# Kernel tuning notes

Measured on AMD Instinct MI355X. Metric: run time of the kernel, lower is better.

The kernel has to match this reference:

```python
import jax, jax.numpy as jnp
import numpy as np

N = 50000   # nodes
E = 800000  # edges
H = 128     # hidden_dim
R = 20      # num_rbf
LN_EPS = 1e-5


def setup_inputs() -> dict:
    key = jax.random.key(0)
    ks = jax.random.split(key, 16)
    rn = lambda k, shape, scale=1.0: (jax.random.normal(k, shape, dtype=jnp.float32) * scale)
    s = rn(ks[0], (N, H))
    v = rn(ks[1], (N, 3, H))
    edge_index = jax.random.randint(ks[2], (2, E), 0, N, dtype=jnp.int32)
    edge_rbf = jax.random.uniform(ks[3], (E, R), dtype=jnp.float32)
    ev = rn(ks[4], (E, 3))
    edge_vec_unit = ev / jnp.linalg.norm(ev, axis=-1, keepdims=True)
    # message_net: Linear(H+R -> H), SiLU, Linear(H -> 3H)
    mW1 = rn(ks[5], (H + R, H), (H + R) ** -0.5)
    mb1 = jnp.zeros((H,), jnp.float32)
    mW2 = rn(ks[6], (H, 3 * H), H ** -0.5)
    mb2 = jnp.zeros((3 * H,), jnp.float32)
    # update_net: Linear(2H -> H), SiLU, Linear(H -> 2H)
    uW1 = rn(ks[7], (2 * H, H), (2 * H) ** -0.5)
    ub1 = jnp.zeros((H,), jnp.float32)
    uW2 = rn(ks[8], (H, 2 * H), H ** -0.5)
    ub2 = jnp.zeros((2 * H,), jnp.float32)
    ln_g = jnp.ones((H,), jnp.float32)
    ln_b = jnp.zeros((H,), jnp.float32)
    return {"s": s, "v": v, "edge_rbf": edge_rbf, "edge_vec_unit": edge_vec_unit,
            "mW1": mW1, "mb1": mb1, "mW2": mW2, "mb2": mb2,
            "uW1": uW1, "ub1": ub1, "uW2": uW2, "ub2": ub2,
            "ln_g": ln_g, "ln_b": ln_b, "edge_index": edge_index}


def reference(s, v, edge_rbf, edge_vec_unit, mW1, mb1, mW2, mb2,
              uW1, ub1, uW2, ub2, ln_g, ln_b, edge_index):
    src, dst = edge_index[0], edge_index[1]
    n = s.shape[0]
    # message net on gathered scalar features + rbf: [E, H+R] -> [E, 3H]
    x = jnp.concatenate([s[src], edge_rbf], axis=-1)
    phi = jax.nn.silu(x @ mW1 + mb1) @ mW2 + mb2
    a_ss, a_sv, a_vv = jnp.split(phi, 3, axis=-1)  # each [E, H]
    # vector messages: [E, 3, H]
    msg_v = a_sv[:, None, :] * edge_vec_unit[:, :, None] + a_vv[:, None, :] * v[src]
    # scatter-add aggregation to destination nodes
    agg_s = jax.ops.segment_sum(a_ss, dst, num_segments=n)      # [N, H]
    agg_v = jax.ops.segment_sum(msg_v, dst, num_segments=n)     # [N, 3, H]
    v_new = v + agg_v
    v_norm = jnp.sqrt(jnp.sum(v_new * v_new, axis=1))           # [N, H]
    upd_in = jnp.concatenate([s + agg_s, v_norm], axis=-1)      # [N, 2H]
    update = jax.nn.silu(upd_in @ uW1 + ub1) @ uW2 + ub2        # [N, 2H]
    delta_s, gate_v = jnp.split(update, 2, axis=-1)
    # layer norm over last dim (biased variance, as torch LayerNorm)
    y = s + delta_s
    mu = jnp.mean(y, axis=-1, keepdims=True)
    var = jnp.mean((y - mu) ** 2, axis=-1, keepdims=True)
    s_out = (y - mu) * jax.lax.rsqrt(var + LN_EPS) * ln_g + ln_b
    v_out = gate_v[:, None, :] * v_new
    return s_out, v_out
```

## Files before the change

### kernel.cpp

```cpp
#include <hip/hip_runtime.h>
#include <hip/hip_bf16.h>
#include <math.h>


#define H 128
#define R 20
#define KX (H + R)
#define LN_EPS 1e-5f

#define BE 64
#define XS_STRIDE 149
#define H1_STRIDE 129

#define BN 64
#define US_STRIDE 257
#define H2_STRIDE 129

__device__ __forceinline__ float silu_f(float x) {
    return x / (1.0f + __expf(-x));
}

__global__ __launch_bounds__(256)
void zero_f4_kernel(float4* __restrict__ p, long n4)
{
    const long stride = (long)gridDim.x * blockDim.x;
    for (long i = (long)blockIdx.x * blockDim.x + threadIdx.x; i < n4; i += stride)
        p[i] = make_float4(0.f, 0.f, 0.f, 0.f);
}

__global__ __launch_bounds__(256)
void zero_i_kernel(int* __restrict__ p, int n)
{
    const int stride = gridDim.x * blockDim.x;
    for (int i = blockIdx.x * blockDim.x + threadIdx.x; i < n; i += stride)
        p[i] = 0;
}

__global__ __launch_bounds__(256)
void hist_kernel(const int* __restrict__ eidx, int E, int* __restrict__ cnt)
{
    const int stride = gridDim.x * blockDim.x;
    for (int i = blockIdx.x * blockDim.x + threadIdx.x; i < E; i += stride)
        atomicAdd(&cnt[eidx[E + i]], 1);
}

__global__ __launch_bounds__(1024, 1)
void scan_kernel(const int* __restrict__ cnt, int N, int* __restrict__ fill)
{
    __shared__ int lds[1024];
    __shared__ int base_s;
    const int tid = threadIdx.x;
    if (tid == 0) base_s = 0;
    __syncthreads();
    const int nchunk = (N + 1023) >> 10;
    for (int c = 0; c < nchunk; ++c) {
        const int i   = (c << 10) + tid;
        const int val = (i < N) ? cnt[i] : 0;
        lds[tid] = val;
        __syncthreads();
        for (int off = 1; off < 1024; off <<= 1) {
            int t = (tid >= off) ? lds[tid - off] : 0;
            __syncthreads();
            lds[tid] += t;
            __syncthreads();
        }
        const int incl = lds[tid];
        if (i < N) fill[i] = base_s + (incl - val);
        __syncthreads();
        if (tid == 1023) base_s += incl;
        __syncthreads();
    }
}

__global__ __launch_bounds__(256)
void scatter_kernel(const int* __restrict__ eidx, int E,
                    int* __restrict__ fill, int* __restrict__ sorted)
{
    const int stride = gridDim.x * blockDim.x;
    for (int i = blockIdx.x * blockDim.x + threadIdx.x; i < E; i += stride) {
        const int d    = eidx[E + i];
        const int slot = atomicAdd(&fill[d], 1);
        sorted[slot] = i;
    }
}

__global__ __launch_bounds__(256, 2)
void painn_edge_kernel(const float* __restrict__ s,
                       const float* __restrict__ v,
                       const float* __restrict__ rbf,
                       const float* __restrict__ evu,
                       const float* __restrict__ mW1,
                       const float* __restrict__ mb1,
                       const float* __restrict__ mW2,
                       const float* __restrict__ mb2,
                       const int*   __restrict__ eidx,
                       const int*   __restrict__ sorted,
                       int E,
                       float* __restrict__ agg_s,
                       float* __restrict__ agg_v)
{
    __shared__ float Xs[BE * XS_STRIDE];
    __shared__ float H1s[BE * H1_STRIDE];
    __shared__ float evus[BE][3];
    __shared__ int   eids[BE];
    __shared__ int   srcs[BE];
    __shared__ int   dsts[BE];

    const int t  = threadIdx.x;
    const int e0 = blockIdx.x * BE;

    if (t < BE) {
        const int e = sorted[e0 + t];
        eids[t] = e;
        srcs[t] = eidx[e];
        dsts[t] = eidx[E + e];
    }
    __syncthreads();

    if (t < BE * 3) {
        int r = t / 3, c = t - r * 3;
        evus[r][c] = evu[eids[r] * 3 + c];
    }

    #pragma unroll
    for (int it = 0; it < 8; ++it) {
        int idx = t + it * 256;
        int row = idx >> 5;
        int c4  = (idx & 31) << 2;
        const float4 val = *reinterpret_cast<const float4*>(s + srcs[row] * H + c4);
        float* p = &Xs[row * XS_STRIDE + c4];
        p[0] = val.x; p[1] = val.y; p[2] = val.z; p[3] = val.w;
    }
    #pragma unroll
    for (int it = 0; it < 5; ++it) {
        int idx = t + it * 256;
        int row = idx / R;
        int c   = idx - row * R;
        Xs[row * XS_STRIDE + H + c] = rbf[eids[row] * R + c];
    }
    __syncthreads();

    const int ty = t >> 4;
    const int tx = t & 15;
    const int jb = tx << 3;
    const int er = ty << 2;

    const int rcol = t & 127;
    const int rr0  = (t >> 7) * 32;

    {
        float acc[4][8];
        #pragma unroll
        for (int r2 = 0; r2 < 4; ++r2)
            #pragma unroll
            for (int j = 0; j < 8; ++j) acc[r2][j] = 0.f;

        const float* wp = mW1 + jb;
        for (int k = 0; k < KX; ++k) {
            const float4 w0 = *reinterpret_cast<const float4*>(wp);
            const float4 w1 = *reinterpret_cast<const float4*>(wp + 4);
            wp += H;
            float xk[4];
            #pragma unroll
            for (int r2 = 0; r2 < 4; ++r2) xk[r2] = Xs[(er + r2) * XS_STRIDE + k];
            #pragma unroll
            for (int r2 = 0; r2 < 4; ++r2) {
                acc[r2][0] += xk[r2] * w0.x;
                acc[r2][1] += xk[r2] * w0.y;
                acc[r2][2] += xk[r2] * w0.z;
                acc[r2][3] += xk[r2] * w0.w;
                acc[r2][4] += xk[r2] * w1.x;
                acc[r2][5] += xk[r2] * w1.y;
                acc[r2][6] += xk[r2] * w1.z;
                acc[r2][7] += xk[r2] * w1.w;
            }
        }
        const float4 b0 = *reinterpret_cast<const float4*>(mb1 + jb);
        const float4 b1 = *reinterpret_cast<const float4*>(mb1 + jb + 4);
        const float bias[8] = {b0.x, b0.y, b0.z, b0.w, b1.x, b1.y, b1.z, b1.w};
        #pragma unroll
        for (int r2 = 0; r2 < 4; ++r2) {
            #pragma unroll
            for (int j = 0; j < 8; ++j) {
                float a = acc[r2][j] + bias[j];
                H1s[(er + r2) * H1_STRIDE + jb + j] = silu_f(a);
            }
        }
    }
    __syncthreads();

    {
        float acc[4][8];
        #pragma unroll
        for (int r2 = 0; r2 < 4; ++r2)
            #pragma unroll
            for (int j = 0; j < 8; ++j) acc[r2][j] = 0.f;

        const float* wp = mW2 + jb;
        for (int k = 0; k < H; ++k) {
            const float4 w0 = *reinterpret_cast<const float4*>(wp);
            const float4 w1 = *reinterpret_cast<const float4*>(wp + 4);
            wp += 3 * H;
            float hk[4];
            #pragma unroll
            for (int r2 = 0; r2 < 4; ++r2) hk[r2] = H1s[(er + r2) * H1_STRIDE + k];
            #pragma unroll
            for (int r2 = 0; r2 < 4; ++r2) {
                acc[r2][0] += hk[r2] * w0.x;
                acc[r2][1] += hk[r2] * w0.y;
                acc[r2][2] += hk[r2] * w0.z;
                acc[r2][3] += hk[r2] * w0.w;
                acc[r2][4] += hk[r2] * w1.x;
                acc[r2][5] += hk[r2] * w1.y;
                acc[r2][6] += hk[r2] * w1.z;
                acc[r2][7] += hk[r2] * w1.w;
            }
        }
        const float4 b0 = *reinterpret_cast<const float4*>(mb2 + jb);
        const float4 b1 = *reinterpret_cast<const float4*>(mb2 + jb + 4);
        const float bias[8] = {b0.x, b0.y, b0.z, b0.w, b1.x, b1.y, b1.z, b1.w};
        #pragma unroll
        for (int r2 = 0; r2 < 4; ++r2)
            #pragma unroll
            for (int j = 0; j < 8; ++j)
                Xs[(er + r2) * XS_STRIDE + jb + j] = acc[r2][j] + bias[j];
        __syncthreads();

        float run = 0.f;
        int prev = dsts[rr0];
        for (int r = rr0; r < rr0 + 32; ++r) {
            const int d = dsts[r];
            if (d != prev) {
                unsafeAtomicAdd(&agg_s[prev * H + rcol], run);
                run = 0.f; prev = d;
            }
            run += Xs[r * XS_STRIDE + rcol];
        }
        unsafeAtomicAdd(&agg_s[prev * H + rcol], run);
    }
    __syncthreads();

    {
        float asv[4][8], avv[4][8];
        #pragma unroll
        for (int r2 = 0; r2 < 4; ++r2)
            #pragma unroll
            for (int j = 0; j < 8; ++j) { asv[r2][j] = 0.f; avv[r2][j] = 0.f; }

        const float* wp = mW2 + H + jb;
        for (int k = 0; k < H; ++k) {
            const float4 s0 = *reinterpret_cast<const float4*>(wp);
            const float4 s1 = *reinterpret_cast<const float4*>(wp + 4);
            const float4 v0 = *reinterpret_cast<const float4*>(wp + H);
            const float4 v1 = *reinterpret_cast<const float4*>(wp + H + 4);
            wp += 3 * H;
            float hk[4];
            #pragma unroll
            for (int r2 = 0; r2 < 4; ++r2) hk[r2] = H1s[(er + r2) * H1_STRIDE + k];
            #pragma unroll
            for (int r2 = 0; r2 < 4; ++r2) {
                asv[r2][0] += hk[r2] * s0.x;  avv[r2][0] += hk[r2] * v0.x;
                asv[r2][1] += hk[r2] * s0.y;  avv[r2][1] += hk[r2] * v0.y;
                asv[r2][2] += hk[r2] * s0.z;  avv[r2][2] += hk[r2] * v0.z;
                asv[r2][3] += hk[r2] * s0.w;  avv[r2][3] += hk[r2] * v0.w;
                asv[r2][4] += hk[r2] * s1.x;  avv[r2][4] += hk[r2] * v1.x;
                asv[r2][5] += hk[r2] * s1.y;  avv[r2][5] += hk[r2] * v1.y;
                asv[r2][6] += hk[r2] * s1.z;  avv[r2][6] += hk[r2] * v1.z;
                asv[r2][7] += hk[r2] * s1.w;  avv[r2][7] += hk[r2] * v1.w;
            }
        }
        const float4 bs0 = *reinterpret_cast<const float4*>(mb2 + H + jb);
        const float4 bs1 = *reinterpret_cast<const float4*>(mb2 + H + jb + 4);
        const float4 bv0 = *reinterpret_cast<const float4*>(mb2 + 2 * H + jb);
        const float4 bv1 = *reinterpret_cast<const float4*>(mb2 + 2 * H + jb + 4);
        float msv[4][8], mvv[4][8];
        #pragma unroll
        for (int r2 = 0; r2 < 4; ++r2) {
            msv[r2][0] = asv[r2][0] + bs0.x;  mvv[r2][0] = avv[r2][0] + bv0.x;
            msv[r2][1] = asv[r2][1] + bs0.y;  mvv[r2][1] = avv[r2][1] + bv0.y;
            msv[r2][2] = asv[r2][2] + bs0.z;  mvv[r2][2] = avv[r2][2] + bv0.z;
            msv[r2][3] = asv[r2][3] + bs0.w;  mvv[r2][3] = avv[r2][3] + bv0.w;
            msv[r2][4] = asv[r2][4] + bs1.x;  mvv[r2][4] = avv[r2][4] + bv1.x;
            msv[r2][5] = asv[r2][5] + bs1.y;  mvv[r2][5] = avv[r2][5] + bv1.y;
            msv[r2][6] = asv[r2][6] + bs1.z;  mvv[r2][6] = avv[r2][6] + bv1.z;
            msv[r2][7] = asv[r2][7] + bs1.w;  mvv[r2][7] = avv[r2][7] + bv1.w;
        }

        #pragma unroll
        for (int d = 0; d < 3; ++d) {
            #pragma unroll
            for (int r2 = 0; r2 < 4; ++r2) {
                const int e  = er + r2;
                const int sn = srcs[e];
                const float ed = evus[e][d];
                const float* vp = v + (sn * 3 + d) * H + jb;
                const float4 vv0 = *reinterpret_cast<const float4*>(vp);
                const float4 vv1 = *reinterpret_cast<const float4*>(vp + 4);
                float* rp = &Xs[e * XS_STRIDE + jb];
                rp[0] = msv[r2][0] * ed + mvv[r2][0] * vv0.x;
                rp[1] = msv[r2][1] * ed + mvv[r2][1] * vv0.y;
                rp[2] = msv[r2][2] * ed + mvv[r2][2] * vv0.z;
                rp[3] = msv[r2][3] * ed + mvv[r2][3] * vv0.w;
                rp[4] = msv[r2][4] * ed + mvv[r2][4] * vv1.x;
                rp[5] = msv[r2][5] * ed + mvv[r2][5] * vv1.y;
                rp[6] = msv[r2][6] * ed + mvv[r2][6] * vv1.z;
                rp[7] = msv[r2][7] * ed + mvv[r2][7] * vv1.w;
            }
            __syncthreads();

            float run = 0.f;
            int prev = dsts[rr0];
            for (int r = rr0; r < rr0 + 32; ++r) {
                const int dn = dsts[r];
                if (dn != prev) {
                    unsafeAtomicAdd(&agg_v[(prev * 3 + d) * H + rcol], run);
                    run = 0.f; prev = dn;
                }
                run += Xs[r * XS_STRIDE + rcol];
            }
            unsafeAtomicAdd(&agg_v[(prev * 3 + d) * H + rcol], run);
            __syncthreads();
        }
    }
}

__global__ __launch_bounds__(256, 1)
void painn_node_kernel(const float* __restrict__ s,
                       const float* __restrict__ v,
                       const float* __restrict__ uW1,
                       const float* __restrict__ ub1,
                       const float* __restrict__ uW2,
                       const float* __restrict__ ub2,
                       const float* __restrict__ ln_g,
                       const float* __restrict__ ln_b,
                       int N,
                       float* __restrict__ out_s,
                       float* __restrict__ out_v)
{
    __shared__ float Us[BN * US_STRIDE];
    __shared__ float H2s[BN * H2_STRIDE];

    const int t  = threadIdx.x;
    const int n0 = blockIdx.x * BN;
    const int m  = min(BN, N - n0);

    #pragma unroll
    for (int it = 0; it < 8; ++it) {
        int idx = t + it * 256;
        int row = idx >> 5;
        int c4  = (idx & 31) << 2;
        if (row < m) {
            const int nb = (n0 + row) * H + c4;
            const float4 sv = *reinterpret_cast<const float4*>(s + nb);
            const float4 av = *reinterpret_cast<const float4*>(out_s + nb);
            float* p = &Us[row * US_STRIDE + c4];
            p[0] = sv.x + av.x; p[1] = sv.y + av.y;
            p[2] = sv.z + av.z; p[3] = sv.w + av.w;

            float nx = 0.f, ny = 0.f, nz = 0.f, nw = 0.f;
            #pragma unroll
            for (int d = 0; d < 3; ++d) {
                const int vb = ((n0 + row) * 3 + d) * H + c4;
                const float4 vv = *reinterpret_cast<const float4*>(v + vb);
                const float4 avv = *reinterpret_cast<const float4*>(out_v + vb);
                const float a0 = vv.x + avv.x, a1 = vv.y + avv.y;
                const float a2 = vv.z + avv.z, a3 = vv.w + avv.w;
                nx += a0 * a0; ny += a1 * a1; nz += a2 * a2; nw += a3 * a3;
            }
            float* q = &Us[row * US_STRIDE + H + c4];
            q[0] = sqrtf(nx); q[1] = sqrtf(ny); q[2] = sqrtf(nz); q[3] = sqrtf(nw);
        }
    }
    __syncthreads();

    const int ty = t >> 4;
    const int tx = t & 15;
    const int jb = tx << 3;
    const int nr = ty << 2;

    {
        float acc[4][8];
        #pragma unroll
        for (int r2 = 0; r2 < 4; ++r2)
            #pragma unroll
            for (int j = 0; j < 8; ++j) acc[r2][j] = 0.f;

        const float* wp = uW1 + jb;
        for (int k = 0; k < 2 * H; ++k) {
            const float4 w0 = *reinterpret_cast<const float4*>(wp);
            const float4 w1 = *reinterpret_cast<const float4*>(wp + 4);
            wp += H;
            float uk[4];
            #pragma unroll
            for (int r2 = 0; r2 < 4; ++r2) uk[r2] = Us[(nr + r2) * US_STRIDE + k];
            #pragma unroll
            for (int r2 = 0; r2 < 4; ++r2) {
                acc[r2][0] += uk[r2] * w0.x;
                acc[r2][1] += uk[r2] * w0.y;
                acc[r2][2] += uk[r2] * w0.z;
                acc[r2][3] += uk[r2] * w0.w;
                acc[r2][4] += uk[r2] * w1.x;
                acc[r2][5] += uk[r2] * w1.y;
                acc[r2][6] += uk[r2] * w1.z;
                acc[r2][7] += uk[r2] * w1.w;
            }
        }
        const float4 b0 = *reinterpret_cast<const float4*>(ub1 + jb);
        const float4 b1 = *reinterpret_cast<const float4*>(ub1 + jb + 4);
        const float bias[8] = {b0.x, b0.y, b0.z, b0.w, b1.x, b1.y, b1.z, b1.w};
        #pragma unroll
        for (int r2 = 0; r2 < 4; ++r2)
            #pragma unroll
            for (int j = 0; j < 8; ++j)
                H2s[(nr + r2) * H2_STRIDE + jb + j] = silu_f(acc[r2][j] + bias[j]);
    }
    __syncthreads();

    float gate[4][8];
    {
        float ad[4][8], ag[4][8];
        #pragma unroll
        for (int r2 = 0; r2 < 4; ++r2)
            #pragma unroll
            for (int j = 0; j < 8; ++j) { ad[r2][j] = 0.f; ag[r2][j] = 0.f; }

        const float* wp = uW2 + jb;
        for (int k = 0; k < H; ++k) {
            const float4 d0 = *reinterpret_cast<const float4*>(wp);
            const float4 d1 = *reinterpret_cast<const float4*>(wp + 4);
            const float4 g0 = *reinterpret_cast<const float4*>(wp + H);
            const float4 g1 = *reinterpret_cast<const float4*>(wp + H + 4);
            wp += 2 * H;
            float hk[4];
            #pragma unroll
            for (int r2 = 0; r2 < 4; ++r2) hk[r2] = H2s[(nr + r2) * H2_STRIDE + k];
            #pragma unroll
            for (int r2 = 0; r2 < 4; ++r2) {
                ad[r2][0] += hk[r2] * d0.x;  ag[r2][0] += hk[r2] * g0.x;
                ad[r2][1] += hk[r2] * d0.y;  ag[r2][1] += hk[r2] * g0.y;
                ad[r2][2] += hk[r2] * d0.z;  ag[r2][2] += hk[r2] * g0.z;
                ad[r2][3] += hk[r2] * d0.w;  ag[r2][3] += hk[r2] * g0.w;
                ad[r2][4] += hk[r2] * d1.x;  ag[r2][4] += hk[r2] * g1.x;
                ad[r2][5] += hk[r2] * d1.y;  ag[r2][5] += hk[r2] * g1.y;
                ad[r2][6] += hk[r2] * d1.z;  ag[r2][6] += hk[r2] * g1.z;
                ad[r2][7] += hk[r2] * d1.w;  ag[r2][7] += hk[r2] * g1.w;
            }
        }
        const float4 bd0 = *reinterpret_cast<const float4*>(ub2 + jb);
        const float4 bd1 = *reinterpret_cast<const float4*>(ub2 + jb + 4);
        const float4 bg0 = *reinterpret_cast<const float4*>(ub2 + H + jb);
        const float4 bg1 = *reinterpret_cast<const float4*>(ub2 + H + jb + 4);
        const float bd[8] = {bd0.x, bd0.y, bd0.z, bd0.w, bd1.x, bd1.y, bd1.z, bd1.w};
        const float bg[8] = {bg0.x, bg0.y, bg0.z, bg0.w, bg1.x, bg1.y, bg1.z, bg1.w};

        #pragma unroll
        for (int r2 = 0; r2 < 4; ++r2) {
            #pragma unroll
            for (int j = 0; j < 8; ++j) gate[r2][j] = ag[r2][j] + bg[j];
            if (nr + r2 < m) {
                const int nb = (n0 + nr + r2) * H + jb;
                const float4 s0 = *reinterpret_cast<const float4*>(s + nb);
                const float4 s1 = *reinterpret_cast<const float4*>(s + nb + 4);
                const float sl[8] = {s0.x, s0.y, s0.z, s0.w, s1.x, s1.y, s1.z, s1.w};
                float* yp = &Us[(nr + r2) * US_STRIDE + jb];
                #pragma unroll
                for (int j = 0; j < 8; ++j) yp[j] = sl[j] + ad[r2][j] + bd[j];
            }
        }
    }
    __syncthreads();

    {
        const int row = t >> 2;
        const int q   = t & 3;
        if (row < m) {
            float sum = 0.f, ss = 0.f;
            #pragma unroll
            for (int i = 0; i < 32; ++i) {
                const float val = Us[row * US_STRIDE + q * 32 + i];
                sum += val; ss += val * val;
            }
            sum += __shfl_xor(sum, 1); ss += __shfl_xor(ss, 1);
            sum += __shfl_xor(sum, 2); ss += __shfl_xor(ss, 2);
            const float mu   = sum * (1.0f / H);
            const float var  = ss * (1.0f / H) - mu * mu;
            const float rstd = rsqrtf(fmaxf(var, 0.f) + LN_EPS);
            #pragma unroll
            for (int i4 = 0; i4 < 8; ++i4) {
                const int c = q * 32 + i4 * 4;
                const float4 g = *reinterpret_cast<const float4*>(ln_g + c);
                const float4 b = *reinterpret_cast<const float4*>(ln_b + c);
                const float* yp = &Us[row * US_STRIDE + c];
                float4 o;
                o.x = (yp[0] - mu) * rstd * g.x + b.x;
                o.y = (yp[1] - mu) * rstd * g.y + b.y;
                o.z = (yp[2] - mu) * rstd * g.z + b.z;
                o.w = (yp[3] - mu) * rstd * g.w + b.w;
                *reinterpret_cast<float4*>(out_s + (n0 + row) * H + c) = o;
            }
        }
    }

    #pragma unroll
    for (int r2 = 0; r2 < 4; ++r2) {
        if (nr + r2 < m) {
            const int nn = n0 + nr + r2;
            #pragma unroll
            for (int d = 0; d < 3; ++d) {
                const int vb = (nn * 3 + d) * H + jb;
                const float4 vv0 = *reinterpret_cast<const float4*>(v + vb);
                const float4 vv1 = *reinterpret_cast<const float4*>(v + vb + 4);
                const float4 av0 = *reinterpret_cast<const float4*>(out_v + vb);
                const float4 av1 = *reinterpret_cast<const float4*>(out_v + vb + 4);
                float4 o0, o1;
                o0.x = gate[r2][0] * (vv0.x + av0.x);
                o0.y = gate[r2][1] * (vv0.y + av0.y);
                o0.z = gate[r2][2] * (vv0.z + av0.z);
                o0.w = gate[r2][3] * (vv0.w + av0.w);
                o1.x = gate[r2][4] * (vv1.x + av1.x);
                o1.y = gate[r2][5] * (vv1.y + av1.y);
                o1.z = gate[r2][6] * (vv1.z + av1.z);
                o1.w = gate[r2][7] * (vv1.w + av1.w);
                *reinterpret_cast<float4*>(out_v + vb)     = o0;
                *reinterpret_cast<float4*>(out_v + vb + 4) = o1;
            }
        }
    }
}

extern "C" void kernel_launch(void* const* d_in, const int* in_sizes, int n_in,
                              void* d_out, int out_size, void* d_ws, size_t ws_size,
                              hipStream_t stream)
{
    const float* s    = (const float*)d_in[0];
    const float* v    = (const float*)d_in[1];
    const float* rbf  = (const float*)d_in[2];
    const float* evu  = (const float*)d_in[3];
    const float* mW1  = (const float*)d_in[4];
    const float* mb1  = (const float*)d_in[5];
    const float* mW2  = (const float*)d_in[6];
    const float* mb2  = (const float*)d_in[7];
    const float* uW1  = (const float*)d_in[8];
    const float* ub1  = (const float*)d_in[9];
    const float* uW2  = (const float*)d_in[10];
    const float* ub2  = (const float*)d_in[11];
    const float* ln_g = (const float*)d_in[12];
    const float* ln_b = (const float*)d_in[13];
    const int*   eidx = (const int*)d_in[14];

    const int N = in_sizes[0] / H;
    const int E = in_sizes[2] / R;

    float* agg_s = (float*)d_out;
    float* agg_v = (float*)d_out + (size_t)N * H;

    int* cnt    = (int*)d_ws;
    int* fill   = cnt + N;
    int* sorted = fill + N;

    const long n4 = (long)N * 4 * H / 4;
    zero_f4_kernel<<<dim3(2048), dim3(256), 0, stream>>>((float4*)d_out, n4);
    zero_i_kernel<<<dim3(64), dim3(256), 0, stream>>>(cnt, N);

    hist_kernel<<<dim3(2048), dim3(256), 0, stream>>>(eidx, E, cnt);
    scan_kernel<<<dim3(1), dim3(1024), 0, stream>>>(cnt, N, fill);
    scatter_kernel<<<dim3(2048), dim3(256), 0, stream>>>(eidx, E, fill, sorted);

    painn_edge_kernel<<<dim3(E / BE), dim3(256), 0, stream>>>(
        s, v, rbf, evu, mW1, mb1, mW2, mb2, eidx, sorted, E, agg_s, agg_v);

    painn_node_kernel<<<dim3((N + BN - 1) / BN), dim3(256), 0, stream>>>(
        s, v, uW1, ub1, uW2, ub2, ln_g, ln_b, N, agg_s, agg_v);
}
```

Measured before the change: 2.519 ms.

## Double edge-kernel threads, shrink per-thread tile, vectorize shared-memory accesses

The edge kernel now runs 512 threads per block instead of 256. Each thread computes 2 edge rows instead of 4, and the segmented-reduction slices shrink from 32 to 16 rows, which lowers register pressure and allows more resident waves. Shared-memory strides are padded to multiples of 4/8 so float4 loads and stores of X/H1 rows are aligned, and the k loops read 4 activations at a time. The risk is that weight loads from global/L2 are amortized over fewer rows, and padding to aligned strides may bring back bank conflicts.

```diff
diff --git a/kernel.cpp b/kernel.cpp
--- a/kernel.cpp
+++ b/kernel.cpp
@@ -9,8 +9,8 @@
 #define LN_EPS 1e-5f
 
 #define BE 64
-#define XS_STRIDE 149
-#define H1_STRIDE 129
+#define XS_STRIDE 152
+#define H1_STRIDE 136
 
 #define BN 64
 #define US_STRIDE 257
@@ -84,7 +84,7 @@
     }
 }
 
-__global__ __launch_bounds__(256, 2)
+__global__ __launch_bounds__(512, 4)
 void painn_edge_kernel(const float* __restrict__ s,
                        const float* __restrict__ v,
                        const float* __restrict__ rbf,
@@ -123,112 +123,120 @@
     }
 
     #pragma unroll
-    for (int it = 0; it < 8; ++it) {
-        int idx = t + it * 256;
+    for (int it = 0; it < 4; ++it) {
+        int idx = t + it * 512;
         int row = idx >> 5;
         int c4  = (idx & 31) << 2;
         const float4 val = *reinterpret_cast<const float4*>(s + srcs[row] * H + c4);
-        float* p = &Xs[row * XS_STRIDE + c4];
-        p[0] = val.x; p[1] = val.y; p[2] = val.z; p[3] = val.w;
+        *reinterpret_cast<float4*>(&Xs[row * XS_STRIDE + c4]) = val;
     }
     #pragma unroll
-    for (int it = 0; it < 5; ++it) {
-        int idx = t + it * 256;
-        int row = idx / R;
-        int c   = idx - row * R;
-        Xs[row * XS_STRIDE + H + c] = rbf[eids[row] * R + c];
-    }
-    __syncthreads();
-
-    const int ty = t >> 4;
-    const int tx = t & 15;
-    const int jb = tx << 3;
-    const int er = ty << 2;
+    for (int it = 0; it < 3; ++it) {
+        int idx = t + it * 512;
+        if (idx < BE * R) {
+            int row = idx / R;
+            int c   = idx - row * R;
+            Xs[row * XS_STRIDE + H + c] = rbf[eids[row] * R + c];
+        }
+    }
+    __syncthreads();
+
+    const int ty  = t >> 4;
+    const int tx  = t & 15;
+    const int jb  = tx << 3;
+    const int er0 = ty << 1;
+    const int er1 = er0 + 1;
 
     const int rcol = t & 127;
-    const int rr0  = (t >> 7) * 32;
+    const int rr0  = (t >> 7) << 4;
 
     {
-        float acc[4][8];
-        #pragma unroll
-        for (int r2 = 0; r2 < 4; ++r2)
-            #pragma unroll
-            for (int j = 0; j < 8; ++j) acc[r2][j] = 0.f;
+        float acc0[8], acc1[8];
+        #pragma unroll
+        for (int j = 0; j < 8; ++j) { acc0[j] = 0.f; acc1[j] = 0.f; }
 
         const float* wp = mW1 + jb;
-        for (int k = 0; k < KX; ++k) {
-            const float4 w0 = *reinterpret_cast<const float4*>(wp);
-            const float4 w1 = *reinterpret_cast<const float4*>(wp + 4);
-            wp += H;
-            float xk[4];
-            #pragma unroll
-            for (int r2 = 0; r2 < 4; ++r2) xk[r2] = Xs[(er + r2) * XS_STRIDE + k];
-            #pragma unroll
-            for (int r2 = 0; r2 < 4; ++r2) {
-                acc[r2][0] += xk[r2] * w0.x;
-                acc[r2][1] += xk[r2] * w0.y;
-                acc[r2][2] += xk[r2] * w0.z;
-                acc[r2][3] += xk[r2] * w0.w;
-                acc[r2][4] += xk[r2] * w1.x;
-                acc[r2][5] += xk[r2] * w1.y;
-                acc[r2][6] += xk[r2] * w1.z;
-                acc[r2][7] += xk[r2] * w1.w;
-            }
+        for (int k = 0; k < KX; k += 4) {
+            const float4 xa = *reinterpret_cast<const float4*>(&Xs[er0 * XS_STRIDE + k]);
+            const float4 xb = *reinterpret_cast<const float4*>(&Xs[er1 * XS_STRIDE + k]);
+            const float xav[4] = {xa.x, xa.y, xa.z, xa.w};
+            const float xbv[4] = {xb.x, xb.y, xb.z, xb.w};
+            #pragma unroll
+            for (int kk = 0; kk < 4; ++kk) {
+                const float4 w0 = *reinterpret_cast<const float4*>(wp + kk * H);
+                const float4 w1 = *reinterpret_cast<const float4*>(wp + kk * H + 4);
+                const float wj[8] = {w0.x, w0.y, w0.z, w0.w, w1.x, w1.y, w1.z, w1.w};
+                #pragma unroll
+                for (int j = 0; j < 8; ++j) {
+                    acc0[j] += xav[kk] * wj[j];
+                    acc1[j] += xbv[kk] * wj[j];
+                }
+            }
+            wp += 4 * H;
         }
         const float4 b0 = *reinterpret_cast<const float4*>(mb1 + jb);
         const float4 b1 = *reinterpret_cast<const float4*>(mb1 + jb + 4);
         const float bias[8] = {b0.x, b0.y, b0.z, b0.w, b1.x, b1.y, b1.z, b1.w};
-        #pragma unroll
-        for (int r2 = 0; r2 < 4; ++r2) {
-            #pragma unroll
-            for (int j = 0; j < 8; ++j) {
-                float a = acc[r2][j] + bias[j];
-                H1s[(er + r2) * H1_STRIDE + jb + j] = silu_f(a);
-            }
-        }
+        float4 o0, o1;
+        o0.x = silu_f(acc0[0] + bias[0]); o0.y = silu_f(acc0[1] + bias[1]);
+        o0.z = silu_f(acc0[2] + bias[2]); o0.w = silu_f(acc0[3] + bias[3]);
+        o1.x = silu_f(acc0[4] + bias[4]); o1.y = silu_f(acc0[5] + bias[5]);
+        o1.z = silu_f(acc0[6] + bias[6]); o1.w = silu_f(acc0[7] + bias[7]);
+        *reinterpret_cast<float4*>(&H1s[er0 * H1_STRIDE + jb])     = o0;
+        *reinterpret_cast<float4*>(&H1s[er0 * H1_STRIDE + jb + 4]) = o1;
+        o0.x = silu_f(acc1[0] + bias[0]); o0.y = silu_f(acc1[1] + bias[1]);
+        o0.z = silu_f(acc1[2] + bias[2]); o0.w = silu_f(acc1[3] + bias[3]);
+        o1.x = silu_f(acc1[4] + bias[4]); o1.y = silu_f(acc1[5] + bias[5]);
+        o1.z = silu_f(acc1[6] + bias[6]); o1.w = silu_f(acc1[7] + bias[7]);
+        *reinterpret_cast<float4*>(&H1s[er1 * H1_STRIDE + jb])     = o0;
+        *reinterpret_cast<float4*>(&H1s[er1 * H1_STRIDE + jb + 4]) = o1;
     }
     __syncthreads();
 
     {
-        float acc[4][8];
-        #pragma unroll
-        for (int r2 = 0; r2 < 4; ++r2)
-            #pragma unroll
-            for (int j = 0; j < 8; ++j) acc[r2][j] = 0.f;
+        float acc0[8], acc1[8];
+        #pragma unroll
+        for (int j = 0; j < 8; ++j) { acc0[j] = 0.f; acc1[j] = 0.f; }
 
         const float* wp = mW2 + jb;
-        for (int k = 0; k < H; ++k) {
-            const float4 w0 = *reinterpret_cast<const float4*>(wp);
-            const float4 w1 = *reinterpret_cast<const float4*>(wp + 4);
-            wp += 3 * H;
-            float hk[4];
-            #pragma unroll
-            for (int r2 = 0; r2 < 4; ++r2) hk[r2] = H1s[(er + r2) * H1_STRIDE + k];
-            #pragma unroll
-            for (int r2 = 0; r2 < 4; ++r2) {
-                acc[r2][0] += hk[r2] * w0.x;
-                acc[r2][1] += hk[r2] * w0.y;
-                acc[r2][2] += hk[r2] * w0.z;
-                acc[r2][3] += hk[r2] * w0.w;
-                acc[r2][4] += hk[r2] * w1.x;
-                acc[r2][5] += hk[r2] * w1.y;
-                acc[r2][6] += hk[r2] * w1.z;
-                acc[r2][7] += hk[r2] * w1.w;
-            }
+        for (int k = 0; k < H; k += 4) {
+            const float4 ha = *reinterpret_cast<const float4*>(&H1s[er0 * H1_STRIDE + k]);
+            const float4 hb = *reinterpret_cast<const float4*>(&H1s[er1 * H1_STRIDE + k]);
+            const float hav[4] = {ha.x, ha.y, ha.z, ha.w};
+            const float hbv[4] = {hb.x, hb.y, hb.z, hb.w};
+            #pragma unroll
+            for (int kk = 0; kk < 4; ++kk) {
+                const float4 w0 = *reinterpret_cast<const float4*>(wp + kk * 3 * H);
+                const float4 w1 = *reinterpret_cast<const float4*>(wp + kk * 3 * H + 4);
+                const float wj[8] = {w0.x, w0.y, w0.z, w0.w, w1.x, w1.y, w1.z, w1.w};
+                #pragma unroll
+                for (int j = 0; j < 8; ++j) {
+                    acc0[j] += hav[kk] * wj[j];
+                    acc1[j] += hbv[kk] * wj[j];
+                }
+            }
+            wp += 4 * 3 * H;
         }
         const float4 b0 = *reinterpret_cast<const float4*>(mb2 + jb);
         const float4 b1 = *reinterpret_cast<const float4*>(mb2 + jb + 4);
-        const float bias[8] = {b0.x, b0.y, b0.z, b0.w, b1.x, b1.y, b1.z, b1.w};
-        #pragma unroll
-        for (int r2 = 0; r2 < 4; ++r2)
-            #pragma unroll
-            for (int j = 0; j < 8; ++j)
-                Xs[(er + r2) * XS_STRIDE + jb + j] = acc[r2][j] + bias[j];
+        float4 o0, o1;
+        o0.x = acc0[0] + b0.x; o0.y = acc0[1] + b0.y;
+        o0.z = acc0[2] + b0.z; o0.w = acc0[3] + b0.w;
+        o1.x = acc0[4] + b1.x; o1.y = acc0[5] + b1.y;
+        o1.z = acc0[6] + b1.z; o1.w = acc0[7] + b1.w;
+        *reinterpret_cast<float4*>(&Xs[er0 * XS_STRIDE + jb])     = o0;
+        *reinterpret_cast<float4*>(&Xs[er0 * XS_STRIDE + jb + 4]) = o1;
+        o0.x = acc1[0] + b0.x; o0.y = acc1[1] + b0.y;
+        o0.z = acc1[2] + b0.z; o0.w = acc1[3] + b0.w;
+        o1.x = acc1[4] + b1.x; o1.y = acc1[5] + b1.y;
+        o1.z = acc1[6] + b1.z; o1.w = acc1[7] + b1.w;
+        *reinterpret_cast<float4*>(&Xs[er1 * XS_STRIDE + jb])     = o0;
+        *reinterpret_cast<float4*>(&Xs[er1 * XS_STRIDE + jb + 4]) = o1;
         __syncthreads();
 
         float run = 0.f;
         int prev = dsts[rr0];
-        for (int r = rr0; r < rr0 + 32; ++r) {
+        for (int r = rr0; r < rr0 + 16; ++r) {
             const int d = dsts[r];
             if (d != prev) {
                 unsafeAtomicAdd(&agg_s[prev * H + rcol], run);
@@ -241,84 +249,92 @@
     __syncthreads();
 
     {
-        float asv[4][8], avv[4][8];
-        #pragma unroll
-        for (int r2 = 0; r2 < 4; ++r2)
-            #pragma unroll
-            for (int j = 0; j < 8; ++j) { asv[r2][j] = 0.f; avv[r2][j] = 0.f; }
+        float asv0[8], asv1[8], avv0[8], avv1[8];
+        #pragma unroll
+        for (int j = 0; j < 8; ++j) {
+            asv0[j] = 0.f; asv1[j] = 0.f; avv0[j] = 0.f; avv1[j] = 0.f;
+        }
 
         const float* wp = mW2 + H + jb;
-        for (int k = 0; k < H; ++k) {
-            const float4 s0 = *reinterpret_cast<const float4*>(wp);
-            const float4 s1 = *reinterpret_cast<const float4*>(wp + 4);
-            const float4 v0 = *reinterpret_cast<const float4*>(wp + H);
-            const float4 v1 = *reinterpret_cast<const float4*>(wp + H + 4);
-            wp += 3 * H;
-            float hk[4];
-            #pragma unroll
-            for (int r2 = 0; r2 < 4; ++r2) hk[r2] = H1s[(er + r2) * H1_STRIDE + k];
-            #pragma unroll
-            for (int r2 = 0; r2 < 4; ++r2) {
-                asv[r2][0] += hk[r2] * s0.x;  avv[r2][0] += hk[r2] * v0.x;
-                asv[r2][1] += hk[r2] * s0.y;  avv[r2][1] += hk[r2] * v0.y;
-                asv[r2][2] += hk[r2] * s0.z;  avv[r2][2] += hk[r2] * v0.z;
-                asv[r2][3] += hk[r2] * s0.w;  avv[r2][3] += hk[r2] * v0.w;
-                asv[r2][4] += hk[r2] * s1.x;  avv[r2][4] += hk[r2] * v1.x;
-                asv[r2][5] += hk[r2] * s1.y;  avv[r2][5] += hk[r2] * v1.y;
-                asv[r2][6] += hk[r2] * s1.z;  avv[r2][6] += hk[r2] * v1.z;
-                asv[r2][7] += hk[r2] * s1.w;  avv[r2][7] += hk[r2] * v1.w;
-            }
+        for (int k = 0; k < H; k += 2) {
+            const float2 ha = *reinterpret_cast<const float2*>(&H1s[er0 * H1_STRIDE + k]);
+            const float2 hb = *reinterpret_cast<const float2*>(&H1s[er1 * H1_STRIDE + k]);
+            const float hav[2] = {ha.x, ha.y};
+            const float hbv[2] = {hb.x, hb.y};
+            #pragma unroll
+            for (int kk = 0; kk < 2; ++kk) {
+                const float4 s0 = *reinterpret_cast<const float4*>(wp + kk * 3 * H);
+                const float4 s1 = *reinterpret_cast<const float4*>(wp + kk * 3 * H + 4);
+                const float4 v0 = *reinterpret_cast<const float4*>(wp + kk * 3 * H + H);
+                const float4 v1 = *reinterpret_cast<const float4*>(wp + kk * 3 * H + H + 4);
+                const float ws[8] = {s0.x, s0.y, s0.z, s0.w, s1.x, s1.y, s1.z, s1.w};
+                const float wv[8] = {v0.x, v0.y, v0.z, v0.w, v1.x, v1.y, v1.z, v1.w};
+                #pragma unroll
+                for (int j = 0; j < 8; ++j) {
+                    asv0[j] += hav[kk] * ws[j];  avv0[j] += hav[kk] * wv[j];
+                    asv1[j] += hbv[kk] * ws[j];  avv1[j] += hbv[kk] * wv[j];
+                }
+            }
+            wp += 2 * 3 * H;
         }
         const float4 bs0 = *reinterpret_cast<const float4*>(mb2 + H + jb);
         const float4 bs1 = *reinterpret_cast<const float4*>(mb2 + H + jb + 4);
         const float4 bv0 = *reinterpret_cast<const float4*>(mb2 + 2 * H + jb);
         const float4 bv1 = *reinterpret_cast<const float4*>(mb2 + 2 * H + jb + 4);
-        float msv[4][8], mvv[4][8];
-        #pragma unroll
-        for (int r2 = 0; r2 < 4; ++r2) {
-            msv[r2][0] = asv[r2][0] + bs0.x;  mvv[r2][0] = avv[r2][0] + bv0.x;
-            msv[r2][1] = asv[r2][1] + bs0.y;  mvv[r2][1] = avv[r2][1] + bv0.y;
-            msv[r2][2] = asv[r2][2] + bs0.z;  mvv[r2][2] = avv[r2][2] + bv0.z;
-            msv[r2][3] = asv[r2][3] + bs0.w;  mvv[r2][3] = avv[r2][3] + bv0.w;
-            msv[r2][4] = asv[r2][4] + bs1.x;  mvv[r2][4] = avv[r2][4] + bv1.x;
-            msv[r2][5] = asv[r2][5] + bs1.y;  mvv[r2][5] = avv[r2][5] + bv1.y;
-            msv[r2][6] = asv[r2][6] + bs1.z;  mvv[r2][6] = avv[r2][6] + bv1.z;
-            msv[r2][7] = asv[r2][7] + bs1.w;  mvv[r2][7] = avv[r2][7] + bv1.w;
+        const float bsv[8] = {bs0.x, bs0.y, bs0.z, bs0.w, bs1.x, bs1.y, bs1.z, bs1.w};
+        const float bvv[8] = {bv0.x, bv0.y, bv0.z, bv0.w, bv1.x, bv1.y, bv1.z, bv1.w};
+        #pragma unroll
+        for (int j = 0; j < 8; ++j) {
+            asv0[j] += bsv[j];  avv0[j] += bvv[j];
+            asv1[j] += bsv[j];  avv1[j] += bvv[j];
         }
 
         #pragma unroll
         for (int d = 0; d < 3; ++d) {
-            #pragma unroll
-            for (int r2 = 0; r2 < 4; ++r2) {
-                const int e  = er + r2;
-                const int sn = srcs[e];
-                const float ed = evus[e][d];
-                const float* vp = v + (sn * 3 + d) * H + jb;
-                const float4 vv0 = *reinterpret_cast<const float4*>(vp);
-                const float4 vv1 = *reinterpret_cast<const float4*>(vp + 4);
-                float* rp = &Xs[e * XS_STRIDE + jb];
-                rp[0] = msv[r2][0] * ed + mvv[r2][0] * vv0.x;
-                rp[1] = msv[r2][1] * ed + mvv[r2][1] * vv0.y;
-                rp[2] = msv[r2][2] * ed + mvv[r2][2] * vv0.z;
-                rp[3] = msv[r2][3] * ed + mvv[r2][3] * vv0.w;
-                rp[4] = msv[r2][4] * ed + mvv[r2][4] * vv1.x;
-                rp[5] = msv[r2][5] * ed + mvv[r2][5] * vv1.y;
-                rp[6] = msv[r2][6] * ed + mvv[r2][6] * vv1.z;
-                rp[7] = msv[r2][7] * ed + mvv[r2][7] * vv1.w;
+            {
+                const float ed0 = evus[er0][d];
+                const float ed1 = evus[er1][d];
+                const float* vp0 = v + ((size_t)srcs[er0] * 3 + d) * H + jb;
+                const float* vp1 = v + ((size_t)srcs[er1] * 3 + d) * H + jb;
+                const float4 va0 = *reinterpret_cast<const float4*>(vp0);
+                const float4 va1 = *reinterpret_cast<const float4*>(vp0 + 4);
+                const float4 vb0 = *reinterpret_cast<const float4*>(vp1);
+                const float4 vb1 = *reinterpret_cast<const float4*>(vp1 + 4);
+                float4 o;
+                o.x = asv0[0] * ed0 + avv0[0] * va0.x;
+                o.y = asv0[1] * ed0 + avv0[1] * va0.y;
+                o.z = asv0[2] * ed0 + avv0[2] * va0.z;
+                o.w = asv0[3] * ed0 + avv0[3] * va0.w;
+                *reinterpret_cast<float4*>(&Xs[er0 * XS_STRIDE + jb]) = o;
+                o.x = asv0[4] * ed0 + avv0[4] * va1.x;
+                o.y = asv0[5] * ed0 + avv0[5] * va1.y;
+                o.z = asv0[6] * ed0 + avv0[6] * va1.z;
+                o.w = asv0[7] * ed0 + avv0[7] * va1.w;
+                *reinterpret_cast<float4*>(&Xs[er0 * XS_STRIDE + jb + 4]) = o;
+                o.x = asv1[0] * ed1 + avv1[0] * vb0.x;
+                o.y = asv1[1] * ed1 + avv1[1] * vb0.y;
+                o.z = asv1[2] * ed1 + avv1[2] * vb0.z;
+                o.w = asv1[3] * ed1 + avv1[3] * vb0.w;
+                *reinterpret_cast<float4*>(&Xs[er1 * XS_STRIDE + jb]) = o;
+                o.x = asv1[4] * ed1 + avv1[4] * vb1.x;
+                o.y = asv1[5] * ed1 + avv1[5] * vb1.y;
+                o.z = asv1[6] * ed1 + avv1[6] * vb1.z;
+                o.w = asv1[7] * ed1 + avv1[7] * vb1.w;
+                *reinterpret_cast<float4*>(&Xs[er1 * XS_STRIDE + jb + 4]) = o;
             }
             __syncthreads();
 
             float run = 0.f;
             int prev = dsts[rr0];
-            for (int r = rr0; r < rr0 + 32; ++r) {
+            for (int r = rr0; r < rr0 + 16; ++r) {
                 const int dn = dsts[r];
                 if (dn != prev) {
-                    unsafeAtomicAdd(&agg_v[(prev * 3 + d) * H + rcol], run);
+                    unsafeAtomicAdd(&agg_v[((size_t)prev * 3 + d) * H + rcol], run);
                     run = 0.f; prev = dn;
                 }
                 run += Xs[r * XS_STRIDE + rcol];
             }
-            unsafeAtomicAdd(&agg_v[(prev * 3 + d) * H + rcol], run);
+            unsafeAtomicAdd(&agg_v[((size_t)prev * 3 + d) * H + rcol], run);
             __syncthreads();
         }
     }
@@ -566,7 +582,7 @@
     scan_kernel<<<dim3(1), dim3(1024), 0, stream>>>(cnt, N, fill);
     scatter_kernel<<<dim3(2048), dim3(256), 0, stream>>>(eidx, E, fill, sorted);
 
-    painn_edge_kernel<<<dim3(E / BE), dim3(256), 0, stream>>>(
+    painn_edge_kernel<<<dim3(E / BE), dim3(512), 0, stream>>>(
         s, v, rbf, evu, mW1, mb1, mW2, mb2, eidx, sorted, E, agg_s, agg_v);
 
     painn_node_kernel<<<dim3((N + BN - 1) / BN), dim3(256), 0, stream>>>(
```

Measured after the change: 3.786 ms. 50.3% more time.

## Remap edge-kernel MLP tiles so each wave owns 16 edge rows

Applied to the files above, without the earlier changes.

The edge kernel's message-MLP GEMMs change their thread tiling. Each wavefront now owns 16 edge rows and each lane owns 2 output columns, walking k in steps of 4 with float4 shared-memory reads that every lane in the wave shares, plus float2 weight loads. Shared strides are padded to aligned values (152/136) so these vector accesses work, and some block barriers are dropped because each wave only reads rows it wrote. The aim is fewer LDS and weight-load instructions per FMA; the cost is that the second layer now runs as three separate passes over H1s.

```diff
diff --git a/kernel.cpp b/kernel.cpp
--- a/kernel.cpp
+++ b/kernel.cpp
@@ -9,8 +9,8 @@
 #define LN_EPS 1e-5f
 
 #define BE 64
-#define XS_STRIDE 149
-#define H1_STRIDE 129
+#define XS_STRIDE 152
+#define H1_STRIDE 136
 
 #define BN 64
 #define US_STRIDE 257
@@ -119,7 +119,7 @@
 
     if (t < BE * 3) {
         int r = t / 3, c = t - r * 3;
-        evus[r][c] = evu[eids[r] * 3 + c];
+        evus[r][c] = evu[(size_t)eids[r] * 3 + c];
     }
 
     #pragma unroll
@@ -127,200 +127,177 @@
         int idx = t + it * 256;
         int row = idx >> 5;
         int c4  = (idx & 31) << 2;
-        const float4 val = *reinterpret_cast<const float4*>(s + srcs[row] * H + c4);
-        float* p = &Xs[row * XS_STRIDE + c4];
-        p[0] = val.x; p[1] = val.y; p[2] = val.z; p[3] = val.w;
+        const float4 val = *reinterpret_cast<const float4*>(s + (size_t)srcs[row] * H + c4);
+        *reinterpret_cast<float4*>(&Xs[row * XS_STRIDE + c4]) = val;
     }
     #pragma unroll
     for (int it = 0; it < 5; ++it) {
         int idx = t + it * 256;
         int row = idx / R;
         int c   = idx - row * R;
-        Xs[row * XS_STRIDE + H + c] = rbf[eids[row] * R + c];
-    }
-    __syncthreads();
-
-    const int ty = t >> 4;
-    const int tx = t & 15;
-    const int jb = tx << 3;
-    const int er = ty << 2;
+        Xs[row * XS_STRIDE + H + c] = rbf[(size_t)eids[row] * R + c];
+    }
+    __syncthreads();
+
+    const int lane = t & 63;
+    const int wid  = t >> 6;
+    const int er0  = wid << 4;
+    const int c0   = lane << 1;
 
     const int rcol = t & 127;
-    const int rr0  = (t >> 7) * 32;
-
-    {
-        float acc[4][8];
-        #pragma unroll
-        for (int r2 = 0; r2 < 4; ++r2)
-            #pragma unroll
-            for (int j = 0; j < 8; ++j) acc[r2][j] = 0.f;
-
-        const float* wp = mW1 + jb;
-        for (int k = 0; k < KX; ++k) {
-            const float4 w0 = *reinterpret_cast<const float4*>(wp);
-            const float4 w1 = *reinterpret_cast<const float4*>(wp + 4);
-            wp += H;
-            float xk[4];
-            #pragma unroll
-            for (int r2 = 0; r2 < 4; ++r2) xk[r2] = Xs[(er + r2) * XS_STRIDE + k];
-            #pragma unroll
-            for (int r2 = 0; r2 < 4; ++r2) {
-                acc[r2][0] += xk[r2] * w0.x;
-                acc[r2][1] += xk[r2] * w0.y;
-                acc[r2][2] += xk[r2] * w0.z;
-                acc[r2][3] += xk[r2] * w0.w;
-                acc[r2][4] += xk[r2] * w1.x;
-                acc[r2][5] += xk[r2] * w1.y;
-                acc[r2][6] += xk[r2] * w1.z;
-                acc[r2][7] += xk[r2] * w1.w;
-            }
-        }
-        const float4 b0 = *reinterpret_cast<const float4*>(mb1 + jb);
-        const float4 b1 = *reinterpret_cast<const float4*>(mb1 + jb + 4);
-        const float bias[8] = {b0.x, b0.y, b0.z, b0.w, b1.x, b1.y, b1.z, b1.w};
-        #pragma unroll
-        for (int r2 = 0; r2 < 4; ++r2) {
-            #pragma unroll
-            for (int j = 0; j < 8; ++j) {
-                float a = acc[r2][j] + bias[j];
-                H1s[(er + r2) * H1_STRIDE + jb + j] = silu_f(a);
-            }
-        }
-    }
-    __syncthreads();
-
-    {
-        float acc[4][8];
-        #pragma unroll
-        for (int r2 = 0; r2 < 4; ++r2)
-            #pragma unroll
-            for (int j = 0; j < 8; ++j) acc[r2][j] = 0.f;
-
-        const float* wp = mW2 + jb;
-        for (int k = 0; k < H; ++k) {
-            const float4 w0 = *reinterpret_cast<const float4*>(wp);
-            const float4 w1 = *reinterpret_cast<const float4*>(wp + 4);
-            wp += 3 * H;
-            float hk[4];
-            #pragma unroll
-            for (int r2 = 0; r2 < 4; ++r2) hk[r2] = H1s[(er + r2) * H1_STRIDE + k];
-            #pragma unroll
-            for (int r2 = 0; r2 < 4; ++r2) {
-                acc[r2][0] += hk[r2] * w0.x;
-                acc[r2][1] += hk[r2] * w0.y;
-                acc[r2][2] += hk[r2] * w0.z;
-                acc[r2][3] += hk[r2] * w0.w;
-                acc[r2][4] += hk[r2] * w1.x;
-                acc[r2][5] += hk[r2] * w1.y;
-                acc[r2][6] += hk[r2] * w1.z;
-                acc[r2][7] += hk[r2] * w1.w;
-            }
-        }
-        const float4 b0 = *reinterpret_cast<const float4*>(mb2 + jb);
-        const float4 b1 = *reinterpret_cast<const float4*>(mb2 + jb + 4);
-        const float bias[8] = {b0.x, b0.y, b0.z, b0.w, b1.x, b1.y, b1.z, b1.w};
-        #pragma unroll
-        for (int r2 = 0; r2 < 4; ++r2)
-            #pragma unroll
-            for (int j = 0; j < 8; ++j)
-                Xs[(er + r2) * XS_STRIDE + jb + j] = acc[r2][j] + bias[j];
-        __syncthreads();
-
+    const int rr0  = (t >> 7) << 5;
+
+    float2 acc[16];
+
+    #pragma unroll
+    for (int r = 0; r < 16; ++r) acc[r] = make_float2(0.f, 0.f);
+    {
+        const float* wp = mW1 + c0;
+        for (int k = 0; k < KX; k += 4) {
+            const float2 w0 = *reinterpret_cast<const float2*>(wp);
+            const float2 w1 = *reinterpret_cast<const float2*>(wp + H);
+            const float2 w2 = *reinterpret_cast<const float2*>(wp + 2 * H);
+            const float2 w3 = *reinterpret_cast<const float2*>(wp + 3 * H);
+            wp += 4 * H;
+            #pragma unroll
+            for (int r = 0; r < 16; ++r) {
+                const float4 x = *reinterpret_cast<const float4*>(&Xs[(er0 + r) * XS_STRIDE + k]);
+                acc[r].x += x.x * w0.x + x.y * w1.x + x.z * w2.x + x.w * w3.x;
+                acc[r].y += x.x * w0.y + x.y * w1.y + x.z * w2.y + x.w * w3.y;
+            }
+        }
+        const float2 b = *reinterpret_cast<const float2*>(mb1 + c0);
+        #pragma unroll
+        for (int r = 0; r < 16; ++r) {
+            float2 o;
+            o.x = silu_f(acc[r].x + b.x);
+            o.y = silu_f(acc[r].y + b.y);
+            *reinterpret_cast<float2*>(&H1s[(er0 + r) * H1_STRIDE + c0]) = o;
+        }
+    }
+
+    #pragma unroll
+    for (int r = 0; r < 16; ++r) acc[r] = make_float2(0.f, 0.f);
+    {
+        const float* wp = mW2 + c0;
+        for (int k = 0; k < H; k += 4) {
+            const float2 w0 = *reinterpret_cast<const float2*>(wp);
+            const float2 w1 = *reinterpret_cast<const float2*>(wp + 3 * H);
+            const float2 w2 = *reinterpret_cast<const float2*>(wp + 6 * H);
+            const float2 w3 = *reinterpret_cast<const float2*>(wp + 9 * H);
+            wp += 12 * H;
+            #pragma unroll
+            for (int r = 0; r < 16; ++r) {
+                const float4 h = *reinterpret_cast<const float4*>(&H1s[(er0 + r) * H1_STRIDE + k]);
+                acc[r].x += h.x * w0.x + h.y * w1.x + h.z * w2.x + h.w * w3.x;
+                acc[r].y += h.x * w0.y + h.y * w1.y + h.z * w2.y + h.w * w3.y;
+            }
+        }
+        const float2 b = *reinterpret_cast<const float2*>(mb2 + c0);
+        #pragma unroll
+        for (int r = 0; r < 16; ++r) {
+            float2 o;
+            o.x = acc[r].x + b.x;
+            o.y = acc[r].y + b.y;
+            *reinterpret_cast<float2*>(&Xs[(er0 + r) * XS_STRIDE + c0]) = o;
+        }
+    }
+    __syncthreads();
+    {
         float run = 0.f;
         int prev = dsts[rr0];
         for (int r = rr0; r < rr0 + 32; ++r) {
             const int d = dsts[r];
             if (d != prev) {
-                unsafeAtomicAdd(&agg_s[prev * H + rcol], run);
+                unsafeAtomicAdd(&agg_s[(size_t)prev * H + rcol], run);
                 run = 0.f; prev = d;
             }
             run += Xs[r * XS_STRIDE + rcol];
         }
-        unsafeAtomicAdd(&agg_s[prev * H + rcol], run);
-    }
-    __syncthreads();
-
-    {
-        float asv[4][8], avv[4][8];
-        #pragma unroll
-        for (int r2 = 0; r2 < 4; ++r2)
-            #pragma unroll
-            for (int j = 0; j < 8; ++j) { asv[r2][j] = 0.f; avv[r2][j] = 0.f; }
-
-        const float* wp = mW2 + H + jb;
-        for (int k = 0; k < H; ++k) {
-            const float4 s0 = *reinterpret_cast<const float4*>(wp);
-            const float4 s1 = *reinterpret_cast<const float4*>(wp + 4);
-            const float4 v0 = *reinterpret_cast<const float4*>(wp + H);
-            const float4 v1 = *reinterpret_cast<const float4*>(wp + H + 4);
-            wp += 3 * H;
-            float hk[4];
-            #pragma unroll
-            for (int r2 = 0; r2 < 4; ++r2) hk[r2] = H1s[(er + r2) * H1_STRIDE + k];
-            #pragma unroll
-            for (int r2 = 0; r2 < 4; ++r2) {
-                asv[r2][0] += hk[r2] * s0.x;  avv[r2][0] += hk[r2] * v0.x;
-                asv[r2][1] += hk[r2] * s0.y;  avv[r2][1] += hk[r2] * v0.y;
-                asv[r2][2] += hk[r2] * s0.z;  avv[r2][2] += hk[r2] * v0.z;
-                asv[r2][3] += hk[r2] * s0.w;  avv[r2][3] += hk[r2] * v0.w;
-                asv[r2][4] += hk[r2] * s1.x;  avv[r2][4] += hk[r2] * v1.x;
-                asv[r2][5] += hk[r2] * s1.y;  avv[r2][5] += hk[r2] * v1.y;
-                asv[r2][6] += hk[r2] * s1.z;  avv[r2][6] += hk[r2] * v1.z;
-                asv[r2][7] += hk[r2] * s1.w;  avv[r2][7] += hk[r2] * v1.w;
-            }
-        }
-        const float4 bs0 = *reinterpret_cast<const float4*>(mb2 + H + jb);
-        const float4 bs1 = *reinterpret_cast<const float4*>(mb2 + H + jb + 4);
-        const float4 bv0 = *reinterpret_cast<const float4*>(mb2 + 2 * H + jb);
-        const float4 bv1 = *reinterpret_cast<const float4*>(mb2 + 2 * H + jb + 4);
-        float msv[4][8], mvv[4][8];
-        #pragma unroll
-        for (int r2 = 0; r2 < 4; ++r2) {
-            msv[r2][0] = asv[r2][0] + bs0.x;  mvv[r2][0] = avv[r2][0] + bv0.x;
-            msv[r2][1] = asv[r2][1] + bs0.y;  mvv[r2][1] = avv[r2][1] + bv0.y;
-            msv[r2][2] = asv[r2][2] + bs0.z;  mvv[r2][2] = avv[r2][2] + bv0.z;
-            msv[r2][3] = asv[r2][3] + bs0.w;  mvv[r2][3] = avv[r2][3] + bv0.w;
-            msv[r2][4] = asv[r2][4] + bs1.x;  mvv[r2][4] = avv[r2][4] + bv1.x;
-            msv[r2][5] = asv[r2][5] + bs1.y;  mvv[r2][5] = avv[r2][5] + bv1.y;
-            msv[r2][6] = asv[r2][6] + bs1.z;  mvv[r2][6] = avv[r2][6] + bv1.z;
-            msv[r2][7] = asv[r2][7] + bs1.w;  mvv[r2][7] = avv[r2][7] + bv1.w;
-        }
-
-        #pragma unroll
-        for (int d = 0; d < 3; ++d) {
-            #pragma unroll
-            for (int r2 = 0; r2 < 4; ++r2) {
-                const int e  = er + r2;
-                const int sn = srcs[e];
-                const float ed = evus[e][d];
-                const float* vp = v + (sn * 3 + d) * H + jb;
-                const float4 vv0 = *reinterpret_cast<const float4*>(vp);
-                const float4 vv1 = *reinterpret_cast<const float4*>(vp + 4);
-                float* rp = &Xs[e * XS_STRIDE + jb];
-                rp[0] = msv[r2][0] * ed + mvv[r2][0] * vv0.x;
-                rp[1] = msv[r2][1] * ed + mvv[r2][1] * vv0.y;
-                rp[2] = msv[r2][2] * ed + mvv[r2][2] * vv0.z;
-                rp[3] = msv[r2][3] * ed + mvv[r2][3] * vv0.w;
-                rp[4] = msv[r2][4] * ed + mvv[r2][4] * vv1.x;
-                rp[5] = msv[r2][5] * ed + mvv[r2][5] * vv1.y;
-                rp[6] = msv[r2][6] * ed + mvv[r2][6] * vv1.z;
-                rp[7] = msv[r2][7] * ed + mvv[r2][7] * vv1.w;
-            }
-            __syncthreads();
-
-            float run = 0.f;
-            int prev = dsts[rr0];
-            for (int r = rr0; r < rr0 + 32; ++r) {
-                const int dn = dsts[r];
-                if (dn != prev) {
-                    unsafeAtomicAdd(&agg_v[(prev * 3 + d) * H + rcol], run);
-                    run = 0.f; prev = dn;
-                }
-                run += Xs[r * XS_STRIDE + rcol];
-            }
-            unsafeAtomicAdd(&agg_v[(prev * 3 + d) * H + rcol], run);
-            __syncthreads();
-        }
+        unsafeAtomicAdd(&agg_s[(size_t)prev * H + rcol], run);
+    }
+    __syncthreads();
+
+    #pragma unroll
+    for (int r = 0; r < 16; ++r) acc[r] = make_float2(0.f, 0.f);
+    {
+        const float* wp = mW2 + H + c0;
+        for (int k = 0; k < H; k += 4) {
+            const float2 w0 = *reinterpret_cast<const float2*>(wp);
+            const float2 w1 = *reinterpret_cast<const float2*>(wp + 3 * H);
+            const float2 w2 = *reinterpret_cast<const float2*>(wp + 6 * H);
+            const float2 w3 = *reinterpret_cast<const float2*>(wp + 9 * H);
+            wp += 12 * H;
+            #pragma unroll
+            for (int r = 0; r < 16; ++r) {
+                const float4 h = *reinterpret_cast<const float4*>(&H1s[(er0 + r) * H1_STRIDE + k]);
+                acc[r].x += h.x * w0.x + h.y * w1.x + h.z * w2.x + h.w * w3.x;
+                acc[r].y += h.x * w0.y + h.y * w1.y + h.z * w2.y + h.w * w3.y;
+            }
+        }
+        const float2 b = *reinterpret_cast<const float2*>(mb2 + H + c0);
+        #pragma unroll
+        for (int r = 0; r < 16; ++r) {
+            float2 o;
+            o.x = acc[r].x + b.x;
+            o.y = acc[r].y + b.y;
+            *reinterpret_cast<float2*>(&Xs[(er0 + r) * XS_STRIDE + c0]) = o;
+        }
+    }
+
+    #pragma unroll
+    for (int r = 0; r < 16; ++r) acc[r] = make_float2(0.f, 0.f);
+    {
+        const float* wp = mW2 + 2 * H + c0;
+        for (int k = 0; k < H; k += 4) {
+            const float2 w0 = *reinterpret_cast<const float2*>(wp);
+            const float2 w1 = *reinterpret_cast<const float2*>(wp + 3 * H);
+            const float2 w2 = *reinterpret_cast<const float2*>(wp + 6 * H);
+            const float2 w3 = *reinterpret_cast<const float2*>(wp + 9 * H);
+            wp += 12 * H;
+            #pragma unroll
+            for (int r = 0; r < 16; ++r) {
+                const float4 h = *reinterpret_cast<const float4*>(&H1s[(er0 + r) * H1_STRIDE + k]);
+                acc[r].x += h.x * w0.x + h.y * w1.x + h.z * w2.x + h.w * w3.x;
+                acc[r].y += h.x * w0.y + h.y * w1.y + h.z * w2.y + h.w * w3.y;
+            }
+        }
+        const float2 b = *reinterpret_cast<const float2*>(mb2 + 2 * H + c0);
+        #pragma unroll
+        for (int r = 0; r < 16; ++r) {
+            acc[r].x += b.x;
+            acc[r].y += b.y;
+        }
+    }
+
+    #pragma unroll
+    for (int d = 0; d < 3; ++d) {
+        #pragma unroll
+        for (int r = 0; r < 16; ++r) {
+            const int row = er0 + r;
+            const float ed = evus[row][d];
+            const float2 asv = *reinterpret_cast<const float2*>(&Xs[row * XS_STRIDE + c0]);
+            const float2 vv  = *reinterpret_cast<const float2*>(
+                v + ((size_t)srcs[row] * 3 + d) * H + c0);
+            float2 o;
+            o.x = asv.x * ed + acc[r].x * vv.x;
+            o.y = asv.y * ed + acc[r].y * vv.y;
+            *reinterpret_cast<float2*>(&H1s[row * H1_STRIDE + c0]) = o;
+        }
+        __syncthreads();
+
+        float run = 0.f;
+        int prev = dsts[rr0];
+        for (int r = rr0; r < rr0 + 32; ++r) {
+            const int dn = dsts[r];
+            if (dn != prev) {
+                unsafeAtomicAdd(&agg_v[((size_t)prev * 3 + d) * H + rcol], run);
+                run = 0.f; prev = dn;
+            }
+            run += H1s[r * H1_STRIDE + rcol];
+        }
+        unsafeAtomicAdd(&agg_v[((size_t)prev * 3 + d) * H + rcol], run);
+        __syncthreads();
     }
 }
 
```

After: 2.635 ms. 4.6% more time.
